# Performance work log

Hardware: AMD Instinct MI355X
Metric: run time of the kernel (lower is better)

Reference implementation:

```python
import jax, jax.numpy as jnp
import numpy as np

B, S, D, H = 64, 257, 768, 12
HD = D // H            # 64, head dim
GRID = 16              # 16x16 patch grid (S = GRID*GRID + 1)
ADH = 512              # adversarial MLP hidden size
LAMDA = 0.475
EPS = 1e-10


def setup_inputs() -> dict:
    key = jax.random.key(0)
    ks = jax.random.split(key, 12)
    sc = 0.02
    inp = {
        "hidden_states": jax.random.normal(ks[0], (B, S, D), jnp.float32),
        "Wq": jax.random.normal(ks[1], (D, D), jnp.float32) * sc,
        "bq": jnp.zeros((D,), jnp.float32),
        "Wk": jax.random.normal(ks[2], (D, D), jnp.float32) * sc,
        "bk": jnp.zeros((D,), jnp.float32),
        "Wv": jax.random.normal(ks[3], (D, D), jnp.float32) * sc,
        "bv": jnp.zeros((D,), jnp.float32),
        "Wo": jax.random.normal(ks[4], (D, D), jnp.float32) * sc,
        "bo": jnp.zeros((D,), jnp.float32),
        "A1": jax.random.normal(ks[5], (HD, ADH), jnp.float32) * sc,
        "a1": jnp.zeros((ADH,), jnp.float32),
        "A2": jax.random.normal(ks[6], (ADH, 1), jnp.float32) * sc,
        "a2": jnp.zeros((1,), jnp.float32),
        "B1": jax.random.normal(ks[7], (4 * HD, ADH), jnp.float32) * sc,
        "b1": jnp.zeros((ADH,), jnp.float32),
        "B2": jax.random.normal(ks[8], (ADH, 1), jnp.float32) * sc,
        "b2": jnp.zeros((1,), jnp.float32),
    }
    return inp


def _adv_local(feat, W1, c1, W2, c2):
    # feat: [B, H, N, F] -> sigmoid MLP -> [B, H, N]; BCE loss vs target 0 (is_source=False)
    h = jax.nn.relu(jnp.einsum("bhnf,fk->bhnk", feat, W1) + c1)
    p = jax.nn.sigmoid(jnp.einsum("bhnk,ko->bhno", h, W2) + c2)[..., 0]
    loss = -jnp.mean(jnp.log(jnp.clip(1.0 - p, EPS, None)))
    return p, loss


def _merge(patch):
    # patch: [B, H, 256, HD]; vectorized version of the 2x2 block merge loop:
    # merged[r8, c8] = concat(x[2r,2c], x[2r,2c+1], x[2r+1,2c], x[2r+1,2c+1])
    b, h = patch.shape[0], patch.shape[1]
    x = patch.reshape(b, h, GRID // 2, 2, GRID // 2, 2, HD)
    x = x.transpose(0, 1, 2, 4, 3, 5, 6)
    return x.reshape(b, h, (GRID // 2) ** 2, 4 * HD)  # [B, H, 64, 4*HD]


def _out(v):
    # v: [B, H, 64]; vectorized version of out(): nearest-neighbor 8x8 -> 16x16 upsample
    b, h = v.shape[0], v.shape[1]
    g = v.reshape(b, h, 8, 8)
    g = jnp.repeat(jnp.repeat(g, 2, axis=2), 2, axis=3)
    return g.reshape(b, h, 256)


def reference(hidden_states, Wq, bq, Wk, bk, Wv, bv, Wo, bo,
              A1, a1, A2, a2, B1, b1, B2, b2):
    def heads(x):  # [B, S, D] -> [B, H, S, HD]
        return x.reshape(B, S, H, HD).transpose(0, 2, 1, 3)

    q = heads(hidden_states @ Wq + bq)
    k = heads(hidden_states @ Wk + bk)
    v = heads(hidden_states @ Wv + bv)

    scores = jnp.einsum("bhqd,bhkd->bhqk", q, k) / np.sqrt(HD).astype(np.float32)
    probs = jax.nn.softmax(scores, axis=-1)  # [B, H, S, S]

    # posi_emb branch: adversarial entropy reweighting of the CLS query row
    patch = k[:, :, 1:]                       # [B, H, 256, HD]
    merged = _merge(patch)                    # [B, H, 64, 4*HD]
    p2, loss2 = _adv_local(merged, B1, b1, B2, b2)
    output = _out(p2)                         # [B, H, 256]
    p1, loss1 = _adv_local(patch, A1, a1, A2, a2)
    ad_out = (1.0 - LAMDA) * p1 + LAMDA * output
    loss_ad = loss1 + loss2

    entropy = (-ad_out * jnp.log2(ad_out + EPS)
               - (1.0 - ad_out) * jnp.log2(1.0 - ad_out + EPS))   # [B, H, 256]
    entropy = jnp.concatenate(
        [jnp.ones((B, H, 1), probs.dtype), entropy], axis=2)[:, :, None, :]  # [B,H,1,S]
    probs = jnp.concatenate(
        [probs[:, :, 0:1, :] * entropy, probs[:, :, 1:, :]], axis=2)

    ctx = jnp.einsum("bhqk,bhkd->bhqd", probs, v)
    ctx = ctx.transpose(0, 2, 1, 3).reshape(B, S, D)
    attn_out = ctx @ Wo + bo  # dropout rate = 0.0 -> identity
    return attn_out, loss_ad
```

## Files before the change

### kernel.cpp

```cpp
#include <hip/hip_runtime.h>

#define Bb   64
#define Ss   257
#define Hh   12
#define HDd  64
#define Dd   768
#define Mv   16448
#define M2   16512
#define NADH 512

typedef unsigned short u16;
typedef float  f32x4 __attribute__((ext_vector_type(4)));
typedef short  s16x8 __attribute__((ext_vector_type(8)));
typedef short  s16x4 __attribute__((ext_vector_type(4)));

__device__ __forceinline__ float bf2f(u16 u) {
  unsigned x = ((unsigned)u) << 16;
  return __builtin_bit_cast(float, x);
}
__device__ __forceinline__ u16 f2bf(float f) {
  unsigned x = __builtin_bit_cast(unsigned, f);
  x = x + 0x7fffu + ((x >> 16) & 1u);
  return (u16)(x >> 16);
}

__global__ void k_conv_hidden(const float* __restrict__ src, u16* __restrict__ dst) {
  size_t i4 = (size_t)blockIdx.x * 256 + threadIdx.x;
  size_t e = i4 * 4;
  size_t row = e / Dd;
  float4 v = make_float4(0.f, 0.f, 0.f, 0.f);
  if (row < Mv) v = *(const float4*)(src + e);
  ushort4 o;
  o.x = f2bf(v.x); o.y = f2bf(v.y); o.z = f2bf(v.z); o.w = f2bf(v.w);
  *(ushort4*)(dst + e) = o;
}

__global__ void k_tconv(const float* __restrict__ W, u16* __restrict__ Wt,
                        int K, int N) {
  __shared__ float tile[32][33];
  const int tx = threadIdx.x & 31, ty = threadIdx.x >> 5;
  const int n0 = blockIdx.x * 32, k0 = blockIdx.y * 32;
#pragma unroll
  for (int i = 0; i < 4; ++i)
    tile[ty + i*8][tx] = W[(size_t)(k0 + ty + i*8)*N + n0 + tx];
  __syncthreads();
#pragma unroll
  for (int i = 0; i < 4; ++i)
    Wt[(size_t)(n0 + ty + i*8)*K + k0 + tx] = f2bf(tile[tx][ty + i*8]);
}

template<int OUTBF16>
__global__ __launch_bounds__(256) void k_gemm(
    const u16* __restrict__ A, const u16* __restrict__ Bt,
    const float* __restrict__ bias, void* __restrict__ Cout,
    int Mvalid, const float* lossbuf, float* lossout)
{
  const int N = Dd, K = Dd;
  __shared__ u16 As[128*32];
  __shared__ u16 Bs[128*32];
  const int tid = threadIdx.x;
  const int lane = tid & 63, wave = tid >> 6;
  const int m0 = blockIdx.x * 128, n0 = blockIdx.y * 128;

  if (lossout && blockIdx.x == 0 && blockIdx.y == 0 && tid == 0)
    lossout[0] = lossbuf[0];

  const int arow0 = tid >> 2,        auc = tid & 3;
  const int arow1 = (tid >> 2) + 64;
  const u16* agp0 = A  + (size_t)(m0 + arow0) * K + auc * 8;
  const u16* agp1 = A  + (size_t)(m0 + arow1) * K + auc * 8;
  const u16* bgp0 = Bt + (size_t)(n0 + arow0) * K + auc * 8;
  const u16* bgp1 = Bt + (size_t)(n0 + arow1) * K + auc * 8;
  u16* asp0 = As + (arow0*4 + (auc ^ (arow0 & 3))) * 8;
  u16* asp1 = As + (arow1*4 + (auc ^ (arow1 & 3))) * 8;
  u16* bsp0 = Bs + (arow0*4 + (auc ^ (arow0 & 3))) * 8;
  u16* bsp1 = Bs + (arow1*4 + (auc ^ (arow1 & 3))) * 8;

  f32x4 acc[4][4];
#pragma unroll
  for (int i = 0; i < 4; ++i)
#pragma unroll
    for (int j = 0; j < 4; ++j) acc[i][j] = f32x4{0.f, 0.f, 0.f, 0.f};

  const int wr = wave >> 1, wc = wave & 1;
  const int fr = lane & 15, g = lane >> 4;
  const s16x8* afp[4];
  const s16x8* bfp[4];
#pragma unroll
  for (int mi = 0; mi < 4; ++mi) {
    const int rowa = wr*64 + mi*16 + fr;
    afp[mi] = (const s16x8*)(As + (rowa*4 + (g ^ (rowa & 3))) * 8);
    const int rowb = wc*64 + mi*16 + fr;
    bfp[mi] = (const s16x8*)(Bs + (rowb*4 + (g ^ (rowb & 3))) * 8);
  }

  s16x8 ra0 = *(const s16x8*)agp0;
  s16x8 ra1 = *(const s16x8*)agp1;
  s16x8 rb0 = *(const s16x8*)bgp0;
  s16x8 rb1 = *(const s16x8*)bgp1;

  for (int kt = 0; kt < K/32; ++kt) {
    __syncthreads();
    *(s16x8*)asp0 = ra0; *(s16x8*)asp1 = ra1;
    *(s16x8*)bsp0 = rb0; *(s16x8*)bsp1 = rb1;
    __syncthreads();
    if (kt + 1 < K/32) {
      const int o = (kt + 1) * 32;
      ra0 = *(const s16x8*)(agp0 + o);
      ra1 = *(const s16x8*)(agp1 + o);
      rb0 = *(const s16x8*)(bgp0 + o);
      rb1 = *(const s16x8*)(bgp1 + o);
    }
    s16x8 af[4], bf[4];
#pragma unroll
    for (int mi = 0; mi < 4; ++mi) af[mi] = afp[mi][0];
#pragma unroll
    for (int ni = 0; ni < 4; ++ni) bf[ni] = bfp[ni][0];
#pragma unroll
    for (int mi = 0; mi < 4; ++mi)
#pragma unroll
      for (int ni = 0; ni < 4; ++ni)
        acc[mi][ni] = __builtin_amdgcn_mfma_f32_16x16x32_bf16(af[mi], bf[ni], acc[mi][ni], 0, 0, 0);
  }

#pragma unroll
  for (int ni = 0; ni < 4; ++ni) {
    const int col = n0 + wc*64 + ni*16 + fr;
    const float bv = bias[col];
#pragma unroll
    for (int mi = 0; mi < 4; ++mi) {
      const int rowb = m0 + wr*64 + mi*16 + (lane >> 4)*4;
#pragma unroll
      for (int r = 0; r < 4; ++r) {
        const int row = rowb + r;
        if (row < Mvalid) {
          const float vv = acc[mi][ni][r] + bv;
          if (OUTBF16) ((u16*)Cout)[(size_t)row*N + col] = f2bf(vv);
          else         ((float*)Cout)[(size_t)row*N + col] = vv;
        }
      }
    }
  }
}

__global__ __launch_bounds__(256) void k_adv2(
    const u16* __restrict__ kbf,
    const u16* __restrict__ A1t, const float* __restrict__ a1,
    const float* __restrict__ A2, const float* __restrict__ a2,
    const u16* __restrict__ B1t, const float* __restrict__ b1,
    const float* __restrict__ B2, const float* __restrict__ b2,
    float* __restrict__ ent, float* __restrict__ lossacc)
{
  __shared__ u16  pb[2048*8];
  __shared__ float p1s[256], l1s[256];
  __shared__ float s2part[4*64];
  __shared__ float p2s[64], l2s[64];
  __shared__ float red[256];

  const int tid = threadIdx.x;
  const int lane = tid & 63, wave = tid >> 6;
  const int fr = lane & 15, g = lane >> 4;
  const int bh = blockIdx.x;
  const int b = bh / Hh, h = bh % Hh;
  const size_t base = (size_t)b * Ss * Dd + (size_t)h * HDd;

#pragma unroll
  for (int it = 0; it < 8; ++it) {
    const int u = it*256 + tid;
    const int row = u >> 3, c = u & 7;
    const s16x8 v = *(const s16x8*)(kbf + base + (size_t)(1 + row)*Dd + c*8);
    *(s16x8*)(pb + (row*8 + (c ^ (row & 7)))*8) = v;
  }
  __syncthreads();

  {
    s16x8 af[4][2];
#pragma unroll
    for (int mi = 0; mi < 4; ++mi)
#pragma unroll
      for (int kt = 0; kt < 2; ++kt) {
        const int row = wave*64 + mi*16 + fr;
        const int c = kt*4 + g;
        af[mi][kt] = *(const s16x8*)(pb + (row*8 + (c ^ (row & 7)))*8);
      }
    float sp[4][4];
#pragma unroll
    for (int mi = 0; mi < 4; ++mi)
#pragma unroll
      for (int r = 0; r < 4; ++r) sp[mi][r] = 0.f;

    for (int ni = 0; ni < 32; ++ni) {
      const int col = ni*16 + fr;
      f32x4 acc[4];
#pragma unroll
      for (int mi = 0; mi < 4; ++mi) acc[mi] = f32x4{0.f,0.f,0.f,0.f};
#pragma unroll
      for (int kt = 0; kt < 2; ++kt) {
        const s16x8 bfr = *(const s16x8*)(A1t + (size_t)col*64 + kt*32 + g*8);
#pragma unroll
        for (int mi = 0; mi < 4; ++mi)
          acc[mi] = __builtin_amdgcn_mfma_f32_16x16x32_bf16(af[mi][kt], bfr, acc[mi], 0, 0, 0);
      }
      const float c1v = a1[col], w2 = A2[col];
#pragma unroll
      for (int mi = 0; mi < 4; ++mi)
#pragma unroll
        for (int r = 0; r < 4; ++r)
          sp[mi][r] += fmaxf(acc[mi][r] + c1v, 0.f) * w2;
    }
#pragma unroll
    for (int mi = 0; mi < 4; ++mi)
#pragma unroll
      for (int r = 0; r < 4; ++r) {
        float v = sp[mi][r];
        v += __shfl_xor(v, 1); v += __shfl_xor(v, 2);
        v += __shfl_xor(v, 4); v += __shfl_xor(v, 8);
        if (fr == 0) {
          const int row = wave*64 + mi*16 + g*4 + r;
          const float z1 = v + a2[0];
          const float q = 1.f / (1.f + __expf(z1));
          p1s[row] = 1.f - q;
          l1s[row] = -__logf(fmaxf(q, 1e-10f));
        }
      }
  }

#pragma unroll
  for (int pass = 0; pass < 2; ++pass) {
    s16x8 am[2][8];
#pragma unroll
    for (int mi = 0; mi < 2; ++mi)
#pragma unroll
      for (int kt2 = 0; kt2 < 8; ++kt2) {
        const int m = (pass*2 + mi)*16 + fr;
        const int p = kt2 >> 1;
        const int prow = (m >> 3)*32 + (m & 7)*2 + (p >> 1)*16 + (p & 1);
        const int c = (kt2 & 1)*4 + g;
        am[mi][kt2] = *(const s16x8*)(pb + (prow*8 + (c ^ (prow & 7)))*8);
      }
    float sp2[2][4];
#pragma unroll
    for (int mi = 0; mi < 2; ++mi)
#pragma unroll
      for (int r = 0; r < 4; ++r) sp2[mi][r] = 0.f;

    for (int ni2 = 0; ni2 < 8; ++ni2) {
      const int col = wave*128 + ni2*16 + fr;
      f32x4 acc[2];
#pragma unroll
      for (int mi = 0; mi < 2; ++mi) acc[mi] = f32x4{0.f,0.f,0.f,0.f};
#pragma unroll
      for (int kt2 = 0; kt2 < 8; ++kt2) {
        const s16x8 bfr = *(const s16x8*)(B1t + (size_t)col*256 + kt2*32 + g*8);
#pragma unroll
        for (int mi = 0; mi < 2; ++mi)
          acc[mi] = __builtin_amdgcn_mfma_f32_16x16x32_bf16(am[mi][kt2], bfr, acc[mi], 0, 0, 0);
      }
      const float c1v = b1[col], w2 = B2[col];
#pragma unroll
      for (int mi = 0; mi < 2; ++mi)
#pragma unroll
        for (int r = 0; r < 4; ++r)
          sp2[mi][r] += fmaxf(acc[mi][r] + c1v, 0.f) * w2;
    }
#pragma unroll
    for (int mi = 0; mi < 2; ++mi)
#pragma unroll
      for (int r = 0; r < 4; ++r) {
        float v = sp2[mi][r];
        v += __shfl_xor(v, 1); v += __shfl_xor(v, 2);
        v += __shfl_xor(v, 4); v += __shfl_xor(v, 8);
        if (fr == 0) {
          const int m = (pass*2 + mi)*16 + g*4 + r;
          s2part[wave*64 + m] = v;
        }
      }
  }
  __syncthreads();
  if (tid < 64) {
    const float z2 = s2part[tid] + s2part[64 + tid] + s2part[128 + tid]
                   + s2part[192 + tid] + b2[0];
    const float q = 1.f / (1.f + __expf(z2));
    p2s[tid] = 1.f - q;
    l2s[tid] = -__logf(fmaxf(q, 1e-10f));
  }
  __syncthreads();

  const int rr = tid >> 4, cc2 = tid & 15;
  const float p2g = p2s[(rr >> 1)*8 + (cc2 >> 1)];
  const float p1v = p1s[tid];
  const float ad  = 0.525f*p1v + 0.475f*p2g;
  const float entv = -ad*__log2f(ad + 1e-10f) - (1.f - ad)*__log2f(1.f - ad + 1e-10f);
  ent[(size_t)bh*256 + tid] = entv;

  float lc = l1s[tid] * (1.f/196608.f);
  if (tid < 64) lc += l2s[tid] * (1.f/49152.f);
  red[tid] = lc;
  __syncthreads();
  for (int s = 128; s > 0; s >>= 1) {
    if (tid < s) red[tid] += red[tid + s];
    __syncthreads();
  }
  if (tid == 0) atomicAdd(lossacc, red[0]);
}

__global__ __launch_bounds__(256) void k_attn2(
    const u16* __restrict__ qb, const u16* __restrict__ kbf, const u16* __restrict__ vbf,
    const float* __restrict__ entp, u16* __restrict__ ctxb)
{
#define VLD 292
  __shared__ u16 Vt[64*VLD];
  const int tid = threadIdx.x;
  const int lane = tid & 63, wave = tid >> 6;
  const int fr = lane & 15, g = lane >> 4;
  const int bh = blockIdx.x;
  const int b = bh / Hh, h = bh % Hh;
  const size_t base = (size_t)b * Ss * Dd + (size_t)h * HDd;

  for (int c = tid; c < 2304; c += 256) {
    const int k = c >> 3, dc = c & 7;
    s16x8 v = s16x8{0,0,0,0,0,0,0,0};
    if (k < Ss) v = *(const s16x8*)(vbf + base + (size_t)k * Dd + dc * 8);
#pragma unroll
    for (int i = 0; i < 8; ++i) Vt[(dc*8 + i)*VLD + k] = (u16)v[i];
  }
  __syncthreads();

  for (int pi = 0; pi < 5; ++pi) {
    if (pi == 4 && wave != 0) break;
    const int rb = (pi == 4) ? 16 : pi*4 + wave;
    const int q0 = rb * 16;

    const u16* qr = qb + base + (size_t)(q0 + fr)*Dd + g*8;
    const s16x8 qf0 = *(const s16x8*)qr;
    const s16x8 qf1 = *(const s16x8*)(qr + 32);

    f32x4 acc[18];
#pragma unroll
    for (int ct = 0; ct < 18; ++ct) acc[ct] = f32x4{0.f,0.f,0.f,0.f};
#pragma unroll
    for (int ct = 0; ct < 18; ++ct) {
      const u16* kr = kbf + base + (size_t)(ct*16 + fr)*Dd + g*8;
      const s16x8 kf0 = *(const s16x8*)kr;
      const s16x8 kf1 = *(const s16x8*)(kr + 32);
      acc[ct] = __builtin_amdgcn_mfma_f32_16x16x32_bf16(kf0, qf0, acc[ct], 0, 0, 0);
      acc[ct] = __builtin_amdgcn_mfma_f32_16x16x32_bf16(kf1, qf1, acc[ct], 0, 0, 0);
    }

    float mx = -3e38f;
#pragma unroll
    for (int ct = 0; ct < 18; ++ct)
#pragma unroll
      for (int r = 0; r < 4; ++r) {
        const int k = ct*16 + g*4 + r;
        float s = acc[ct][r] * 0.125f;
        if (k >= Ss) s = -1e30f;
        acc[ct][r] = s;
        mx = fmaxf(mx, s);
      }
    mx = fmaxf(mx, __shfl_xor(mx, 16));
    mx = fmaxf(mx, __shfl_xor(mx, 32));
    float sum = 0.f;
#pragma unroll
    for (int ct = 0; ct < 18; ++ct)
#pragma unroll
      for (int r = 0; r < 4; ++r) {
        const float p = __expf(acc[ct][r] - mx);
        acc[ct][r] = p;
        sum += p;
      }
    sum += __shfl_xor(sum, 16);
    sum += __shfl_xor(sum, 32);
    const float inv = 1.f / sum;

    if (rb == 0 && fr == 0) {
#pragma unroll
      for (int ct = 0; ct < 17; ++ct)
#pragma unroll
        for (int r = 0; r < 4; ++r) {
          const int k = ct*16 + g*4 + r;
          if (k > 0 && k < Ss) acc[ct][r] *= entp[(size_t)bh*256 + k - 1];
        }
    }

    unsigned pk[18][2];
#pragma unroll
    for (int ct = 0; ct < 18; ++ct) {
      pk[ct][0] = (unsigned)f2bf(acc[ct][0]*inv) | ((unsigned)f2bf(acc[ct][1]*inv) << 16);
      pk[ct][1] = (unsigned)f2bf(acc[ct][2]*inv) | ((unsigned)f2bf(acc[ct][3]*inv) << 16);
    }

    f32x4 o[4];
#pragma unroll
    for (int dt = 0; dt < 4; ++dt) o[dt] = f32x4{0.f,0.f,0.f,0.f};

#pragma unroll
    for (int kt = 0; kt < 9; ++kt) {
      const unsigned au0 = pk[2*kt][0], au1 = pk[2*kt][1];
      const unsigned au2 = pk[2*kt+1][0], au3 = pk[2*kt+1][1];
      s16x8 af;
      af[0] = (short)(au0 & 0xffff); af[1] = (short)(au0 >> 16);
      af[2] = (short)(au1 & 0xffff); af[3] = (short)(au1 >> 16);
      af[4] = (short)(au2 & 0xffff); af[5] = (short)(au2 >> 16);
      af[6] = (short)(au3 & 0xffff); af[7] = (short)(au3 >> 16);
#pragma unroll
      for (int dt = 0; dt < 4; ++dt) {
        const int hw = (dt*16 + fr)*VLD + kt*32 + g*4;
        const s16x4 lo = *(const s16x4*)(Vt + hw);
        const s16x4 hi = *(const s16x4*)(Vt + hw + 16);
        const s16x8 bf = {lo[0],lo[1],lo[2],lo[3],hi[0],hi[1],hi[2],hi[3]};
        o[dt] = __builtin_amdgcn_mfma_f32_16x16x32_bf16(af, bf, o[dt], 0, 0, 0);
      }
    }

#pragma unroll
    for (int r = 0; r < 4; ++r) {
      const int row = q0 + g*4 + r;
      if (row < Ss) {
#pragma unroll
        for (int dt = 0; dt < 4; ++dt)
          ctxb[base + (size_t)row*Dd + dt*16 + fr] = f2bf(o[dt][r]);
      }
    }
  }
#undef VLD
}

extern "C" void kernel_launch(void* const* d_in, const int* in_sizes, int n_in,
                              void* d_out, int out_size, void* d_ws, size_t ws_size,
                              hipStream_t stream) {
  const float* hid = (const float*)d_in[0];
  const float* Wq  = (const float*)d_in[1];
  const float* bq  = (const float*)d_in[2];
  const float* Wk  = (const float*)d_in[3];
  const float* bk  = (const float*)d_in[4];
  const float* Wv  = (const float*)d_in[5];
  const float* bv  = (const float*)d_in[6];
  const float* Wo  = (const float*)d_in[7];
  const float* bo  = (const float*)d_in[8];
  const float* A1  = (const float*)d_in[9];
  const float* a1  = (const float*)d_in[10];
  const float* A2  = (const float*)d_in[11];
  const float* a2  = (const float*)d_in[12];
  const float* B1  = (const float*)d_in[13];
  const float* b1  = (const float*)d_in[14];
  const float* B2  = (const float*)d_in[15];
  const float* b2  = (const float*)d_in[16];

  char* p = (char*)d_ws;
  size_t off = 0;
  auto alloc = [&](size_t bytes) -> void* {
    void* r = p + off; off += (bytes + 255) & ~(size_t)255; return r;
  };
  u16*   hb   = (u16*)  alloc((size_t)M2*Dd*2);
  u16*   wqt  = (u16*)  alloc((size_t)Dd*Dd*2);
  u16*   wkt  = (u16*)  alloc((size_t)Dd*Dd*2);
  u16*   wvt  = (u16*)  alloc((size_t)Dd*Dd*2);
  u16*   wot  = (u16*)  alloc((size_t)Dd*Dd*2);
  u16*   qbb  = (u16*)  alloc((size_t)M2*Dd*2);
  u16*   kb   = (u16*)  alloc((size_t)M2*Dd*2);
  u16*   vb   = (u16*)  alloc((size_t)M2*Dd*2);
  u16*   ctxb = (u16*)  alloc((size_t)M2*Dd*2);
  float* entw = (float*)alloc((size_t)Bb*Hh*256*4);
  float* lossw = (float*)alloc(256);
  u16*   a1tb = (u16*)  alloc((size_t)NADH*HDd*2);
  u16*   b1tb = (u16*)  alloc((size_t)NADH*4*HDd*2);

  hipMemsetAsync(lossw, 0, 4, stream);
  k_conv_hidden<<<dim3((M2*Dd/4)/256), 256, 0, stream>>>(hid, hb);
  dim3 tg(24, 24);
  k_tconv<<<tg, 256, 0, stream>>>(Wq, wqt, Dd, Dd);
  k_tconv<<<tg, 256, 0, stream>>>(Wk, wkt, Dd, Dd);
  k_tconv<<<tg, 256, 0, stream>>>(Wv, wvt, Dd, Dd);
  k_tconv<<<tg, 256, 0, stream>>>(Wo, wot, Dd, Dd);
  k_tconv<<<dim3(16, 2), 256, 0, stream>>>(A1, a1tb, HDd, NADH);
  k_tconv<<<dim3(16, 8), 256, 0, stream>>>(B1, b1tb, 4*HDd, NADH);
  dim3 gg(129, 6);
  k_gemm<1><<<gg, 256, 0, stream>>>(hb, wqt, bq, qbb, Mv, nullptr, nullptr);
  k_gemm<1><<<gg, 256, 0, stream>>>(hb, wkt, bk, kb, Mv, nullptr, nullptr);
  k_gemm<1><<<gg, 256, 0, stream>>>(hb, wvt, bv, vb, Mv, nullptr, nullptr);
  k_adv2<<<Bb*Hh, 256, 0, stream>>>(kb, a1tb, a1, A2, a2, b1tb, b1, B2, b2, entw, lossw);
  k_attn2<<<Bb*Hh, 256, 0, stream>>>(qbb, kb, vb, entw, ctxb);
  k_gemm<0><<<gg, 256, 0, stream>>>(ctxb, wot, bo, (float*)d_out, Mv,
                                    lossw, ((float*)d_out) + (size_t)Mv*Dd);
}
```

Baseline: 570.3 us.

## Use direct global-to-LDS loads in GEMM and split adversarial kernel per half-head

The GEMM now loads A/B tiles with global_load_lds straight into LDS in an unswizzled row layout, replacing the register-staged prefetch that overlapped the next tile's loads with MFMA work. The adversarial MLP kernel is split into two blocks per (batch, head), each covering 128 patches, doubling grid size and caching the bias/weight vectors in LDS. The GEMM change removes register staging but also drops the software prefetch overlap, and its plain row layout may cause LDS bank conflicts on fragment reads.

```diff
diff --git a/kernel.cpp b/kernel.cpp
--- a/kernel.cpp
+++ b/kernel.cpp
@@ -22,6 +22,11 @@
   unsigned x = __builtin_bit_cast(unsigned, f);
   x = x + 0x7fffu + ((x >> 16) & 1u);
   return (u16)(x >> 16);
+}
+__device__ __forceinline__ void gload_lds16(const void* g, void* l) {
+  __builtin_amdgcn_global_load_lds(
+      (const __attribute__((address_space(1))) void*)g,
+      (__attribute__((address_space(3))) void*)l, 16, 0, 0);
 }
 
 __global__ void k_conv_hidden(const float* __restrict__ src, u16* __restrict__ dst) {
@@ -65,16 +70,17 @@
   if (lossout && blockIdx.x == 0 && blockIdx.y == 0 && tid == 0)
     lossout[0] = lossbuf[0];
 
-  const int arow0 = tid >> 2,        auc = tid & 3;
-  const int arow1 = (tid >> 2) + 64;
-  const u16* agp0 = A  + (size_t)(m0 + arow0) * K + auc * 8;
-  const u16* agp1 = A  + (size_t)(m0 + arow1) * K + auc * 8;
-  const u16* bgp0 = Bt + (size_t)(n0 + arow0) * K + auc * 8;
-  const u16* bgp1 = Bt + (size_t)(n0 + arow1) * K + auc * 8;
-  u16* asp0 = As + (arow0*4 + (auc ^ (arow0 & 3))) * 8;
-  u16* asp1 = As + (arow1*4 + (auc ^ (arow1 & 3))) * 8;
-  u16* bsp0 = Bs + (arow0*4 + (auc ^ (arow0 & 3))) * 8;
-  u16* bsp1 = Bs + (arow1*4 + (auc ^ (arow1 & 3))) * 8;
+  const int c0 = wave*2, c1 = wave*2 + 1;
+  const int r0 = c0*16 + (lane >> 2), r1 = c1*16 + (lane >> 2);
+  const int u8 = (lane & 3) * 8;
+  const u16* gA0 = A  + (size_t)(m0 + r0)*K + u8;
+  const u16* gA1 = A  + (size_t)(m0 + r1)*K + u8;
+  const u16* gB0 = Bt + (size_t)(n0 + r0)*K + u8;
+  const u16* gB1 = Bt + (size_t)(n0 + r1)*K + u8;
+  u16* lA0 = As + c0*512;
+  u16* lA1 = As + c1*512;
+  u16* lB0 = Bs + c0*512;
+  u16* lB1 = Bs + c1*512;
 
   f32x4 acc[4][4];
 #pragma unroll
@@ -88,29 +94,18 @@
   const s16x8* bfp[4];
 #pragma unroll
   for (int mi = 0; mi < 4; ++mi) {
-    const int rowa = wr*64 + mi*16 + fr;
-    afp[mi] = (const s16x8*)(As + (rowa*4 + (g ^ (rowa & 3))) * 8);
-    const int rowb = wc*64 + mi*16 + fr;
-    bfp[mi] = (const s16x8*)(Bs + (rowb*4 + (g ^ (rowb & 3))) * 8);
-  }
-
-  s16x8 ra0 = *(const s16x8*)agp0;
-  s16x8 ra1 = *(const s16x8*)agp1;
-  s16x8 rb0 = *(const s16x8*)bgp0;
-  s16x8 rb1 = *(const s16x8*)bgp1;
+    afp[mi] = (const s16x8*)(As + (wr*64 + mi*16 + fr)*32 + g*8);
+    bfp[mi] = (const s16x8*)(Bs + (wc*64 + mi*16 + fr)*32 + g*8);
+  }
 
   for (int kt = 0; kt < K/32; ++kt) {
+    const int o = kt * 32;
     __syncthreads();
-    *(s16x8*)asp0 = ra0; *(s16x8*)asp1 = ra1;
-    *(s16x8*)bsp0 = rb0; *(s16x8*)bsp1 = rb1;
+    gload_lds16(gA0 + o, lA0);
+    gload_lds16(gA1 + o, lA1);
+    gload_lds16(gB0 + o, lB0);
+    gload_lds16(gB1 + o, lB1);
     __syncthreads();
-    if (kt + 1 < K/32) {
-      const int o = (kt + 1) * 32;
-      ra0 = *(const s16x8*)(agp0 + o);
-      ra1 = *(const s16x8*)(agp1 + o);
-      rb0 = *(const s16x8*)(bgp0 + o);
-      rb1 = *(const s16x8*)(bgp1 + o);
-    }
     s16x8 af[4], bf[4];
 #pragma unroll
     for (int mi = 0; mi < 4; ++mi) af[mi] = afp[mi][0];
@@ -129,7 +124,7 @@
     const float bv = bias[col];
 #pragma unroll
     for (int mi = 0; mi < 4; ++mi) {
-      const int rowb = m0 + wr*64 + mi*16 + (lane >> 4)*4;
+      const int rowb = m0 + wr*64 + mi*16 + g*4;
 #pragma unroll
       for (int r = 0; r < 4; ++r) {
         const int row = rowb + r;
@@ -143,7 +138,7 @@
   }
 }
 
-__global__ __launch_bounds__(256) void k_adv2(
+__global__ __launch_bounds__(256) void k_adv3(
     const u16* __restrict__ kbf,
     const u16* __restrict__ A1t, const float* __restrict__ a1,
     const float* __restrict__ A2, const float* __restrict__ a2,
@@ -151,72 +146,78 @@
     const float* __restrict__ B2, const float* __restrict__ b2,
     float* __restrict__ ent, float* __restrict__ lossacc)
 {
-  __shared__ u16  pb[2048*8];
-  __shared__ float p1s[256], l1s[256];
-  __shared__ float s2part[4*64];
-  __shared__ float p2s[64], l2s[64];
+  __shared__ u16  pb[1024*8];
+  __shared__ float ab1[512], aw2[512], bb1[512], bw2[512];
+  __shared__ float p1s[128], l1s[128];
+  __shared__ float s2part[4*32];
+  __shared__ float p2s[32], l2s[32];
   __shared__ float red[256];
 
   const int tid = threadIdx.x;
   const int lane = tid & 63, wave = tid >> 6;
   const int fr = lane & 15, g = lane >> 4;
-  const int bh = blockIdx.x;
+  const int bid = blockIdx.x;
+  const int bh = bid >> 1, half = bid & 1;
   const int b = bh / Hh, h = bh % Hh;
   const size_t base = (size_t)b * Ss * Dd + (size_t)h * HDd;
 
 #pragma unroll
-  for (int it = 0; it < 8; ++it) {
+  for (int it = 0; it < 4; ++it) {
     const int u = it*256 + tid;
     const int row = u >> 3, c = u & 7;
-    const s16x8 v = *(const s16x8*)(kbf + base + (size_t)(1 + row)*Dd + c*8);
+    const s16x8 v = *(const s16x8*)(kbf + base + (size_t)(1 + half*128 + row)*Dd + c*8);
     *(s16x8*)(pb + (row*8 + (c ^ (row & 7)))*8) = v;
   }
+  for (int i = tid; i < 512; i += 256) {
+    ab1[i] = a1[i]; aw2[i] = A2[i]; bb1[i] = b1[i]; bw2[i] = B2[i];
+  }
   __syncthreads();
 
   {
-    s16x8 af[4][2];
-#pragma unroll
-    for (int mi = 0; mi < 4; ++mi)
+    s16x8 af[2][2];
+#pragma unroll
+    for (int mi = 0; mi < 2; ++mi)
 #pragma unroll
       for (int kt = 0; kt < 2; ++kt) {
-        const int row = wave*64 + mi*16 + fr;
+        const int row = wave*32 + mi*16 + fr;
         const int c = kt*4 + g;
         af[mi][kt] = *(const s16x8*)(pb + (row*8 + (c ^ (row & 7)))*8);
       }
-    float sp[4][4];
-#pragma unroll
-    for (int mi = 0; mi < 4; ++mi)
+    float sp[2][4];
+#pragma unroll
+    for (int mi = 0; mi < 2; ++mi)
 #pragma unroll
       for (int r = 0; r < 4; ++r) sp[mi][r] = 0.f;
 
+#pragma unroll 2
     for (int ni = 0; ni < 32; ++ni) {
       const int col = ni*16 + fr;
-      f32x4 acc[4];
-#pragma unroll
-      for (int mi = 0; mi < 4; ++mi) acc[mi] = f32x4{0.f,0.f,0.f,0.f};
+      f32x4 acc[2];
+#pragma unroll
+      for (int mi = 0; mi < 2; ++mi) acc[mi] = f32x4{0.f,0.f,0.f,0.f};
 #pragma unroll
       for (int kt = 0; kt < 2; ++kt) {
         const s16x8 bfr = *(const s16x8*)(A1t + (size_t)col*64 + kt*32 + g*8);
 #pragma unroll
-        for (int mi = 0; mi < 4; ++mi)
+        for (int mi = 0; mi < 2; ++mi)
           acc[mi] = __builtin_amdgcn_mfma_f32_16x16x32_bf16(af[mi][kt], bfr, acc[mi], 0, 0, 0);
       }
-      const float c1v = a1[col], w2 = A2[col];
-#pragma unroll
-      for (int mi = 0; mi < 4; ++mi)
+      const float c1v = ab1[col], w2 = aw2[col];
+#pragma unroll
+      for (int mi = 0; mi < 2; ++mi)
 #pragma unroll
         for (int r = 0; r < 4; ++r)
           sp[mi][r] += fmaxf(acc[mi][r] + c1v, 0.f) * w2;
     }
 #pragma unroll
-    for (int mi = 0; mi < 4; ++mi)
+    for (int mi = 0; mi < 2; ++mi)
 #pragma unroll
       for (int r = 0; r < 4; ++r) {
         float v = sp[mi][r];
         v += __shfl_xor(v, 1); v += __shfl_xor(v, 2);
         v += __shfl_xor(v, 4); v += __shfl_xor(v, 8);
         if (fr == 0) {
-          const int row = wave*64 + mi*16 + g*4 + r;
+          const int row = wave*32 + mi*16 + g*4 + r;
           const float z1 = v + a2[0];
           const float q = 1.f / (1.f + __expf(z1));
           p1s[row] = 1.f - q;
@@ -225,14 +226,13 @@
       }
   }
 
-#pragma unroll
-  for (int pass = 0; pass < 2; ++pass) {
+  {
     s16x8 am[2][8];
 #pragma unroll
     for (int mi = 0; mi < 2; ++mi)
 #pragma unroll
       for (int kt2 = 0; kt2 < 8; ++kt2) {
-        const int m = (pass*2 + mi)*16 + fr;
+        const int m = mi*16 + fr;
         const int p = kt2 >> 1;
         const int prow = (m >> 3)*32 + (m & 7)*2 + (p >> 1)*16 + (p & 1);
         const int c = (kt2 & 1)*4 + g;
@@ -256,7 +256,7 @@
         for (int mi = 0; mi < 2; ++mi)
           acc[mi] = __builtin_amdgcn_mfma_f32_16x16x32_bf16(am[mi][kt2], bfr, acc[mi], 0, 0, 0);
       }
-      const float c1v = b1[col], w2 = B2[col];
+      const float c1v = bb1[col], w2 = bw2[col];
 #pragma unroll
       for (int mi = 0; mi < 2; ++mi)
 #pragma unroll
@@ -271,30 +271,32 @@
         v += __shfl_xor(v, 1); v += __shfl_xor(v, 2);
         v += __shfl_xor(v, 4); v += __shfl_xor(v, 8);
         if (fr == 0) {
-          const int m = (pass*2 + mi)*16 + g*4 + r;
-          s2part[wave*64 + m] = v;
+          const int m = mi*16 + g*4 + r;
+          s2part[wave*32 + m] = v;
         }
       }
   }
   __syncthreads();
-  if (tid < 64) {
-    const float z2 = s2part[tid] + s2part[64 + tid] + s2part[128 + tid]
-                   + s2part[192 + tid] + b2[0];
+  if (tid < 32) {
+    const float z2 = s2part[tid] + s2part[32 + tid] + s2part[64 + tid]
+                   + s2part[96 + tid] + b2[0];
     const float q = 1.f / (1.f + __expf(z2));
     p2s[tid] = 1.f - q;
     l2s[tid] = -__logf(fmaxf(q, 1e-10f));
   }
   __syncthreads();
 
-  const int rr = tid >> 4, cc2 = tid & 15;
-  const float p2g = p2s[(rr >> 1)*8 + (cc2 >> 1)];
-  const float p1v = p1s[tid];
-  const float ad  = 0.525f*p1v + 0.475f*p2g;
-  const float entv = -ad*__log2f(ad + 1e-10f) - (1.f - ad)*__log2f(1.f - ad + 1e-10f);
-  ent[(size_t)bh*256 + tid] = entv;
-
-  float lc = l1s[tid] * (1.f/196608.f);
-  if (tid < 64) lc += l2s[tid] * (1.f/49152.f);
+  float lc = 0.f;
+  if (tid < 128) {
+    const int tr = tid >> 4, cc2 = tid & 15;
+    const float p2g = p2s[(tr >> 1)*8 + (cc2 >> 1)];
+    const float p1v = p1s[tid];
+    const float ad  = 0.525f*p1v + 0.475f*p2g;
+    const float entv = -ad*__log2f(ad + 1e-10f) - (1.f - ad)*__log2f(1.f - ad + 1e-10f);
+    ent[(size_t)bh*256 + half*128 + tid] = entv;
+    lc = l1s[tid] * (1.f/196608.f);
+    if (tid < 32) lc += l2s[tid] * (1.f/49152.f);
+  }
   red[tid] = lc;
   __syncthreads();
   for (int s = 128; s > 0; s >>= 1) {
@@ -479,7 +481,7 @@
   k_gemm<1><<<gg, 256, 0, stream>>>(hb, wqt, bq, qbb, Mv, nullptr, nullptr);
   k_gemm<1><<<gg, 256, 0, stream>>>(hb, wkt, bk, kb, Mv, nullptr, nullptr);
   k_gemm<1><<<gg, 256, 0, stream>>>(hb, wvt, bv, vb, Mv, nullptr, nullptr);
-  k_adv2<<<Bb*Hh, 256, 0, stream>>>(kb, a1tb, a1, A2, a2, b1tb, b1, B2, b2, entw, lossw);
+  k_adv3<<<Bb*Hh*2, 256, 0, stream>>>(kb, a1tb, a1, A2, a2, b1tb, b1, B2, b2, entw, lossw);
   k_attn2<<<Bb*Hh, 256, 0, stream>>>(qbb, kb, vb, entw, ctxb);
   k_gemm<0><<<gg, 256, 0, stream>>>(ctxb, wot, bo, (float*)d_out, Mv,
                                     lossw, ((float*)d_out) + (size_t)Mv*Dd);
```

After: 587.6 us. +3.0%, slower.
